# Optimization experiments

Hardware: AMD Instinct MI355X
Metric: run time of the kernel (lower is better)

The kernel has to match this reference:

```python
import jax, jax.numpy as jnp
import numpy as np

B, N, D = 64, 512, 768


def setup_inputs() -> dict:
    key = jax.random.key(0)
    k = jax.random.split(key, 7)
    x = jax.random.normal(k[0], (B, N, D), dtype=jnp.float32)
    adj = jax.random.normal(k[1], (B, N, N), dtype=jnp.float32)
    # additive BERT-style mask: 0 for valid tokens, -10000 for padding
    lengths = jax.random.randint(k[2], (B,), N // 2, N + 1)
    valid = jnp.arange(N)[None, :] < lengths[:, None]          # [B, N]
    mask = jnp.where(valid, 0.0, -10000.0).astype(jnp.float32).reshape(B, 1, 1, N)
    roots_label = (jax.random.uniform(k[3], (B, N)) < 0.1).astype(jnp.float32)
    root_mask = valid.astype(jnp.int32)
    w_root = jax.random.normal(k[4], (D,), dtype=jnp.float32) / np.sqrt(D)
    b_root = jnp.zeros((), dtype=jnp.float32)
    return {"x": x, "adj": adj, "mask": mask, "roots_label": roots_label,
            "root_mask": root_mask, "w_root": w_root, "b_root": b_root}


def _matrix_tree_multi(scores, root):
    # scores: [B,N,N], root: [B,N]
    A = jnp.exp(scores)
    R = jnp.exp(root)
    L = jnp.sum(A, axis=1)                     # column sums (torch dim=1)
    LL = jnp.zeros_like(A).at[:, jnp.arange(A.shape[1]), jnp.arange(A.shape[1])].set(L + R) - A
    # equivalent to diag(L) - A + diag(R); keep diag of -A zeroed by set:
    LL = (jnp.apply_along_axis(jnp.diag, 1, np.zeros((1,))) if False else LL)  # no-op
    LL = jax.vmap(jnp.diag)(L + R) - A + jax.vmap(jnp.diag)(jnp.diagonal(A, axis1=1, axis2=2))
    # Recompute cleanly to match torch exactly: LL = diag(L) - A + diag(R)
    LL = jax.vmap(jnp.diag)(L) - A + jax.vmap(jnp.diag)(R)
    LL_inv = jnp.linalg.inv(LL)                # [B,N,N]
    LL_inv_diag = jnp.diagonal(LL_inv, axis1=1, axis2=2)   # [B,N]
    d0 = R * LL_inv_diag                       # root marginals [B,N]
    tmp1 = A * LL_inv_diag[:, None, :]         # A[i,j] * diag[j]
    tmp2 = A * jnp.swapaxes(LL_inv, 1, 2)      # A[i,j] * LL_inv[j,i]
    d = tmp1 - tmp2                            # edge marginals [B,N,N]
    return d, d0


def reference(x, adj, mask, roots_label, root_mask, w_root, b_root):
    root = jnp.einsum("bnd,d->bn", x, w_root) + b_root          # [B,N]
    m = mask[:, 0] / -10000.0                                    # [B,1,N], 0 valid / 1 pad
    root = jnp.maximum(root - m[:, 0, :] * 50.0, -40.0)
    scores = adj - m * 50.0 - jnp.swapaxes(m, 1, 2) * 50.0
    scores = jnp.maximum(scores, -40.0)
    d, d0 = _matrix_tree_multi(scores, root)
    # BCE root loss
    active = root_mask.reshape(-1) == 1
    labels = jnp.where(active, roots_label.reshape(-1), 0.0).astype(jnp.float32)
    logits = jnp.clip(d0.reshape(-1), 1e-5, 1.0 - 1e-5).astype(jnp.float32)
    bce = -(labels * jnp.log(logits) + (1.0 - labels) * jnp.log(1.0 - logits))
    loss_root = jnp.mean(bce * root_mask.reshape(-1).astype(jnp.float32))
    # attention = d^T with padded key columns zeroed
    attn = jnp.swapaxes(d, 1, 2)
    pad = jnp.broadcast_to(m.astype(bool), scores.shape)         # [B,N,N]
    attn = jnp.where(pad, 0.0, attn)
    context = jnp.matmul(attn, x)                                # [B,N,D]
    return context, d, loss_root
```

## Files before the change

kernel.cpp:

```cpp
#include <hip/hip_runtime.h>
#include <cstdint>
#include <cstddef>

#define BB 64
#define NN 512
#define DD 768
#define KB 64
#define NSTEP (NN/KB)

typedef __bf16 bf16x8 __attribute__((ext_vector_type(8)));
typedef float f32x4 __attribute__((ext_vector_type(4)));
typedef unsigned short us8 __attribute__((ext_vector_type(8)));
typedef double f64x4 __attribute__((ext_vector_type(4)));
typedef double f64x2 __attribute__((ext_vector_type(2)));

__device__ __forceinline__ float aval(float adjv, float mi, float mj) {
    return expf(fmaxf(adjv - 50.f * (mi + mj), -40.f));
}

__device__ __forceinline__ unsigned short f2bf(float v) {
    union { float f; unsigned int u; } c; c.f = v;
    return (unsigned short)((c.u + 0x7fffu + ((c.u >> 16) & 1u)) >> 16);
}
__device__ __forceinline__ float bf2f(unsigned short h) {
    union { unsigned int u; float f; } c; c.u = ((unsigned int)h) << 16;
    return c.f;
}

__device__ __forceinline__ void gl_lds16(const void* g, void* l) {
    __builtin_amdgcn_global_load_lds((const __attribute__((address_space(1))) unsigned int*)g,
                                     (__attribute__((address_space(3))) unsigned int*)l, 16, 0, 0);
}

__global__ void k_root(const float* __restrict__ x, const float* __restrict__ mask,
                       const float* __restrict__ w, const float* __restrict__ br,
                       float* __restrict__ R) {
    int wave = threadIdx.x >> 6, lane = threadIdx.x & 63;
    int row = blockIdx.x * 4 + wave;
    const float* xr = x + (size_t)row * DD;
    float s = 0.f;
#pragma unroll
    for (int k = 0; k < DD / 64; ++k) s += xr[k * 64 + lane] * w[k * 64 + lane];
    for (int off = 32; off; off >>= 1) s += __shfl_down(s, off, 64);
    if (lane == 0) {
        float m = mask[row] * -1e-4f;
        float rv = fmaxf(s + br[0] - 50.f * m, -40.f);
        R[row] = expf(rv);
    }
}

__global__ void k_colsum(const float* __restrict__ adj, const float* __restrict__ mask,
                         double* __restrict__ Lp) {
    int b = blockIdx.x, chunk = blockIdx.y;
    int j = threadIdx.x;
    float mj = mask[b * NN + j] * -1e-4f;
    const float* ab = adj + (size_t)b * NN * NN;
    double acc = 0.0;
    int i0 = chunk * 128;
    for (int i = i0; i < i0 + 128; ++i) {
        float mi = mask[b * NN + i] * -1e-4f;
        acc += (double)aval(ab[(size_t)i * NN + j], mi, mj);
    }
    Lp[((size_t)b * 4 + chunk) * NN + j] = acc;
}

template <typename T>
__global__ void k_build(const float* __restrict__ adj, const float* __restrict__ mask,
                        const float* __restrict__ R, const double* __restrict__ Lp,
                        T* __restrict__ M) {
    int b = blockIdx.x >> 9;
    int r = blockIdx.x & 511;
    int c = threadIdx.x;
    float mr = mask[b * NN + r] * -1e-4f;
    float mc = mask[b * NN + c] * -1e-4f;
    size_t idx = ((size_t)b * NN + r) * NN + c;
    float a = aval(adj[idx], mr, mc);
    T v;
    if (r == c) {
        const double* lp = Lp + (size_t)b * 4 * NN;
        double L = lp[c] + lp[NN + c] + lp[2 * NN + c] + lp[3 * NN + c];
        v = (T)(L - (double)a + (double)R[b * NN + c]);
    } else {
        v = (T)(-a);
    }
    M[idx] = v;
}

template <typename T>
__global__ void k_savecol(const T* __restrict__ M, T* __restrict__ Cb, int k0) {
    int t = threadIdx.x;
    int c = t & 63, rr = t >> 6;
    int row = blockIdx.x * 4 + rr;
    int b = row >> 9, i = row & 511;
    Cb[(size_t)row * KB + c] = M[((size_t)b * NN + i) * NN + k0 + c];
}

template <typename T>
__global__ void k_invblk(const T* __restrict__ M, T* __restrict__ Bb, int k0) {
    __shared__ double pr[KB];
    __shared__ double fv[KB];
    __shared__ double pvt;
    int b = blockIdx.x;
    int r = threadIdx.x & 63, q = threadIdx.x >> 6;
    double a[16];
    const T* Mb = M + ((size_t)b * NN + k0) * NN + k0;
#pragma unroll
    for (int c = 0; c < 16; ++c) a[c] = (double)Mb[(size_t)r * NN + q * 16 + c];
    for (int k = 0; k < KB; ++k) {
        int kq = k >> 4, kc = k & 15;
        if (r == k && q == kq) pvt = a[kc];
        __syncthreads();
        double ip = 1.0 / pvt;
        if (r == k) {
#pragma unroll
            for (int c = 0; c < 16; ++c) a[c] *= ip;
            if (q == kq) a[kc] = ip;
#pragma unroll
            for (int c = 0; c < 16; ++c) pr[q * 16 + c] = a[c];
        }
        if (r != k && q == kq) fv[r] = a[kc];
        __syncthreads();
        if (r != k) {
            double f = fv[r];
#pragma unroll
            for (int c = 0; c < 16; ++c) a[c] -= f * pr[q * 16 + c];
            if (q == kq) a[kc] = -f * ip;
        }
        __syncthreads();
    }
    T* Bo = Bb + (size_t)b * KB * KB;
#pragma unroll
    for (int c = 0; c < 16; ++c) Bo[r * KB + q * 16 + c] = (T)a[c];
}

__global__ __launch_bounds__(256) void k_piv_mfma(double* __restrict__ M,
                                                  const double* __restrict__ Bb, int step) {
    __shared__ double Ms[64][66];
    int o = blockIdx.x;
    int g = (o & 7) * 64 + (o >> 3);
    int b = g >> 3, jt = g & 7;
    int t = threadIdx.x, w = t >> 6, l = t & 63;
    double* Mb = M + (size_t)b * NN * NN;
    double* Pr = Mb + (size_t)(step * 64) * NN;
    const double* Bi = Bb + (size_t)b * KB * KB;
    if (jt == step) {
        for (int i = 0; i < 16; ++i) {
            int c = i * 256 + t;
            int row = c >> 6, col = c & 63;
            Pr[(size_t)row * NN + step * 64 + col] = Bi[row * 64 + col];
        }
        return;
    }
    const double* Mg = Pr + jt * 64;
    for (int i = 0; i < 8; ++i) {
        int c = i * 256 + t;
        int row = c >> 5, ch = c & 31;
        f64x2 v = *(const f64x2*)(Mg + (size_t)row * NN + ch * 2);
        Ms[row][ch * 2] = v[0]; Ms[row][ch * 2 + 1] = v[1];
    }
    __syncthreads();
    int lr = l & 15, lg = l >> 4;
    double a[16];
#pragma unroll
    for (int kk = 0; kk < 16; ++kk) a[kk] = Bi[(w * 16 + lr) * 64 + kk * 4 + lg];
    double* Og = Pr + (size_t)(w * 16) * NN + jt * 64;
#pragma unroll
    for (int cf = 0; cf < 4; ++cf) {
        f64x4 acc = {0., 0., 0., 0.};
#pragma unroll
        for (int kk = 0; kk < 16; ++kk)
            acc = __builtin_amdgcn_mfma_f64_16x16x4f64(a[kk], Ms[kk * 4 + lg][cf * 16 + lr], acc, 0, 0, 0);
#pragma unroll
        for (int r = 0; r < 4; ++r) Og[(size_t)(lg + 4 * r) * NN + cf * 16 + lr] = acc[r];
    }
}

__global__ __launch_bounds__(256) void k_upd2(double* __restrict__ M,
                                              const double* __restrict__ Bb, int step) {
    __shared__ double Ts[64][66];
    int o = blockIdx.x;
    int g = (o & 7) * 112 + (o >> 3);
    int b = g / 14;
    int x = g % 14;
    int it = x >> 1, half = x & 1;
    if (it >= step) ++it;
    int t = threadIdx.x, w = t >> 6, l = t & 63;
    double* Mb = M + (size_t)b * NN * NN;
    {
        const double* Cg = Mb + (size_t)(it * 64) * NN + step * 64;
        for (int i = 0; i < 8; ++i) {
            int c = i * 256 + t;
            int row = c >> 5, ch = c & 31;
            f64x2 v = *(const f64x2*)(Cg + (size_t)row * NN + ch * 2);
            Ts[row][ch * 2] = -v[0]; Ts[row][ch * 2 + 1] = -v[1];
        }
    }
    __syncthreads();
    int lr = l & 15, lg = l >> 4;
    double a[16];
#pragma unroll
    for (int kk = 0; kk < 16; ++kk) a[kk] = Ts[w * 16 + lr][kk * 4 + lg];
    __syncthreads();
    int nj = half ? 3 : 4;
    for (int jj = 0; jj < nj; ++jj) {
        int jtidx = half ? 4 + jj : jj;
        int jt = (jtidx < step) ? jtidx : jtidx + 1;
        const double* Rg = Mb + (size_t)(step * 64) * NN + jt * 64;
        for (int i = 0; i < 8; ++i) {
            int c = i * 256 + t;
            int row = c >> 5, ch = c & 31;
            f64x2 v = *(const f64x2*)(Rg + (size_t)row * NN + ch * 2);
            Ts[row][ch * 2] = v[0]; Ts[row][ch * 2 + 1] = v[1];
        }
        __syncthreads();
        double* Og = Mb + (size_t)(it * 64 + w * 16) * NN + jt * 64;
#pragma unroll
        for (int cf = 0; cf < 4; ++cf) {
            int c0 = cf * 16 + lr;
            f64x4 acc;
#pragma unroll
            for (int r = 0; r < 4; ++r) acc[r] = Og[(size_t)(lg + 4 * r) * NN + c0];
#pragma unroll
            for (int kk = 0; kk < 16; ++kk)
                acc = __builtin_amdgcn_mfma_f64_16x16x4f64(a[kk], Ts[kk * 4 + lg][c0], acc, 0, 0, 0);
#pragma unroll
            for (int r = 0; r < 4; ++r) Og[(size_t)(lg + 4 * r) * NN + c0] = acc[r];
        }
        __syncthreads();
    }
    if (half) {
        const double* Bi = Bb + (size_t)b * KB * KB;
        for (int i = 0; i < 8; ++i) {
            int c = i * 256 + t;
            int row = c >> 5, ch = c & 31;
            f64x2 v = *(const f64x2*)(Bi + row * 64 + ch * 2);
            Ts[row][ch * 2] = v[0]; Ts[row][ch * 2 + 1] = v[1];
        }
        __syncthreads();
        double* Og = Mb + (size_t)(it * 64 + w * 16) * NN + step * 64;
#pragma unroll
        for (int cf = 0; cf < 4; ++cf) {
            int c0 = cf * 16 + lr;
            f64x4 acc = {0., 0., 0., 0.};
#pragma unroll
            for (int kk = 0; kk < 16; ++kk)
                acc = __builtin_amdgcn_mfma_f64_16x16x4f64(a[kk], Ts[kk * 4 + lg][c0], acc, 0, 0, 0);
#pragma unroll
            for (int r = 0; r < 4; ++r) Og[(size_t)(lg + 4 * r) * NN + c0] = acc[r];
        }
    }
}

template <typename T>
__global__ void k_pivrows(T* __restrict__ M, const T* __restrict__ Bb, int k0) {
    __shared__ double Bi[KB][KB];
    __shared__ double Mt[KB][KB + 1];
    int b = blockIdx.x, jt = blockIdx.y * 64;
    const T* Bo = Bb + (size_t)b * KB * KB;
    T* Mb = M + ((size_t)b * NN + k0) * NN;
    int t = threadIdx.x;
    for (int e = t; e < KB * KB; e += 256) {
        int rr = e >> 6, cc = e & 63;
        Bi[rr][cc] = (double)Bo[e];
        Mt[rr][cc] = (double)Mb[(size_t)rr * NN + jt + cc];
    }
    __syncthreads();
    if (blockIdx.y == (unsigned)(k0 >> 6)) {
        for (int e = t; e < KB * KB; e += 256) {
            int rr = e >> 6, cc = e & 63;
            Mb[(size_t)rr * NN + jt + cc] = (T)Bi[rr][cc];
        }
        return;
    }
    int tx = t & 15, ty = t >> 4;
    double acc[4][4] = {};
    for (int k = 0; k < KB; ++k) {
        double av[4], bv[4];
#pragma unroll
        for (int u = 0; u < 4; ++u) { av[u] = Bi[ty * 4 + u][k]; bv[u] = Mt[k][tx * 4 + u]; }
#pragma unroll
        for (int u = 0; u < 4; ++u)
#pragma unroll
            for (int v = 0; v < 4; ++v) acc[u][v] += av[u] * bv[v];
    }
#pragma unroll
    for (int u = 0; u < 4; ++u)
#pragma unroll
        for (int v = 0; v < 4; ++v)
            Mb[(size_t)(ty * 4 + u) * NN + jt + tx * 4 + v] = (T)acc[u][v];
}

template <typename T>
__global__ void k_update(T* __restrict__ M, const T* __restrict__ Cb, int k0) {
    int step = k0 >> 6;
    int it = blockIdx.y;
    if (it == step) return;
    int b = blockIdx.x, jt = blockIdx.z;
    __shared__ double Ct[KB][KB + 1];
    __shared__ double Rt[KB][KB + 1];
    int t = threadIdx.x;
    const T* Cbb = Cb + ((size_t)b * NN + it * 64) * KB;
    const T* Rb  = M + ((size_t)b * NN + k0) * NN + jt * 64;
    for (int e = t; e < KB * KB; e += 256) {
        int rr = e >> 6, cc = e & 63;
        Ct[rr][cc] = (double)Cbb[(size_t)rr * KB + cc];
        Rt[rr][cc] = (double)Rb[(size_t)rr * NN + cc];
    }
    __syncthreads();
    int tx = t & 15, ty = t >> 4;
    double acc[4][4] = {};
    for (int k = 0; k < KB; ++k) {
        double av[4], bv[4];
#pragma unroll
        for (int u = 0; u < 4; ++u) { av[u] = Ct[ty * 4 + u][k]; bv[u] = Rt[k][tx * 4 + u]; }
#pragma unroll
        for (int u = 0; u < 4; ++u)
#pragma unroll
            for (int v = 0; v < 4; ++v) acc[u][v] += av[u] * bv[v];
    }
    T* Mo = M + ((size_t)b * NN + it * 64) * NN + jt * 64;
    bool blockcol = (jt == step);
#pragma unroll
    for (int u = 0; u < 4; ++u) {
        int row = ty * 4 + u;
#pragma unroll
        for (int v = 0; v < 4; ++v) {
            int col = tx * 4 + v;
            double val = (double)Mo[(size_t)row * NN + col] - acc[u][v];
            if (blockcol) val -= Ct[row][col];
            Mo[(size_t)row * NN + col] = (T)val;
        }
    }
}

template <typename T>
__global__ void k_dgloss(const T* __restrict__ M, const float* __restrict__ R,
                         const float* __restrict__ rlab, const int* __restrict__ rmask,
                         double* __restrict__ Dg, float* __restrict__ lossp) {
    int idx = blockIdx.x * 256 + threadIdx.x;
    int b = idx >> 9, n = idx & 511;
    double xv = (double)M[((size_t)b * NN + n) * NN + n];
    Dg[idx] = xv;
    float d0 = R[idx] * (float)xv;
    float lg = fminf(fmaxf(d0, 1e-5f), 1.f - 1e-5f);
    float rm = (float)rmask[idx];
    float lab = (rmask[idx] == 1) ? rlab[idx] : 0.f;
    float bce = -(lab * logf(lg) + (1.f - lab) * logf(1.f - lg));
    __shared__ double sm[256];
    sm[threadIdx.x] = (double)(bce * rm);
    __syncthreads();
    for (int s = 128; s; s >>= 1) {
        if (threadIdx.x < s) sm[threadIdx.x] += sm[threadIdx.x + s];
        __syncthreads();
    }
    if (threadIdx.x == 0) lossp[blockIdx.x] = (float)sm[0];
}

__global__ void k_lossfin(const float* __restrict__ lossp, float* __restrict__ outv) {
    __shared__ double sm[128];
    sm[threadIdx.x] = (double)lossp[threadIdx.x];
    __syncthreads();
    for (int s = 64; s; s >>= 1) {
        if (threadIdx.x < s) sm[threadIdx.x] += sm[threadIdx.x + s];
        __syncthreads();
    }
    if (threadIdx.x == 0) outv[0] = (float)(sm[0] / (double)(BB * NN));
}

template <typename T>
__global__ void k_d(const T* __restrict__ M, const double* __restrict__ Dg,
                    const float* __restrict__ adj, const float* __restrict__ mask,
                    float* __restrict__ dout) {
    int b = blockIdx.x, i0 = blockIdx.y * 64, j0 = blockIdx.z * 64;
    __shared__ double Xt[64][65];
    int t = threadIdx.x, ii = t & 63, jj0 = t >> 6;
    const T* Mb = M + (size_t)b * NN * NN;
    for (int jj = jj0; jj < 64; jj += 4)
        Xt[jj][ii] = (double)Mb[(size_t)(j0 + jj) * NN + i0 + ii];
    __syncthreads();
    int jc = t & 63, ir0 = t >> 6;
    float mj = mask[b * NN + j0 + jc] * -1e-4f;
    double dg = Dg[b * NN + j0 + jc];
    const float* ab = adj + (size_t)b * NN * NN;
    float* db = dout + (size_t)b * NN * NN;
    for (int ir = ir0; ir < 64; ir += 4) {
        int i = i0 + ir;
        float mi = mask[b * NN + i] * -1e-4f;
        float a = aval(ab[(size_t)i * NN + j0 + jc], mi, mj);
        db[(size_t)i * NN + j0 + jc] = a * (float)(dg - Xt[jc][ir]);
    }
}

template <typename T>
__global__ void k_d2(const T* __restrict__ M, const double* __restrict__ Dg,
                     const float* __restrict__ adj, const float* __restrict__ mask,
                     float* __restrict__ dout,
                     unsigned short* __restrict__ ATh, unsigned short* __restrict__ ATl) {
    int b = blockIdx.x, i0 = blockIdx.y * 64, j0 = blockIdx.z * 64;
    __shared__ float Xt[64][65];
    __shared__ float dt[64][65];
    int t = threadIdx.x, ii = t & 63, jj0 = t >> 6;
    const T* Mb = M + (size_t)b * NN * NN;
    for (int jj = jj0; jj < 64; jj += 4)
        Xt[jj][ii] = (float)Mb[(size_t)(j0 + jj) * NN + i0 + ii];
    __syncthreads();
    int jc = t & 63, ir0 = t >> 6;
    float mj = mask[b * NN + j0 + jc] * -1e-4f;
    double dg = Dg[b * NN + j0 + jc];
    const float* ab = adj + (size_t)b * NN * NN;
    float* db = dout + (size_t)b * NN * NN;
    for (int ir = ir0; ir < 64; ir += 4) {
        int i = i0 + ir;
        float mi = mask[b * NN + i] * -1e-4f;
        float a = aval(ab[(size_t)i * NN + j0 + jc], mi, mj);
        float v = a * (float)(dg - (double)Xt[jc][ir]);
        db[(size_t)i * NN + j0 + jc] = v;
        dt[ir][jc] = v;
    }
    __syncthreads();
    int ql = t >> 2, kq = t & 3;
    us8 vh0, vh1, vl0, vl1;
#pragma unroll
    for (int u = 0; u < 16; ++u) {
        int k = kq * 16 + u;
        float mk = mask[b * NN + i0 + k] * -1e-4f;
        float v = (mk > 0.5f) ? 0.f : dt[k][ql];
        unsigned short h = f2bf(v);
        unsigned short lo = f2bf(v - bf2f(h));
        if (u < 8) { vh0[u] = h; vl0[u] = lo; } else { vh1[u - 8] = h; vl1[u - 8] = lo; }
    }
    size_t ao = ((size_t)b * NN + j0 + ql) * NN + i0 + kq * 16;
    *(us8*)&ATh[ao] = vh0; *(us8*)&ATh[ao + 8] = vh1;
    *(us8*)&ATl[ao] = vl0; *(us8*)&ATl[ao + 8] = vl1;
}

__global__ void k_cvt_x(const float* __restrict__ x,
                        unsigned short* __restrict__ XTh, unsigned short* __restrict__ XTl) {
    int b = blockIdx.x, k0 = blockIdx.y * 64, c0 = blockIdx.z * 64;
    __shared__ float xs[64][65];
    int t = threadIdx.x;
#pragma unroll
    for (int rep = 0; rep < 16; ++rep) {
        int e = rep * 256 + t;
        int row = e >> 6, col = e & 63;
        xs[row][col] = x[((size_t)b * NN + k0 + row) * DD + c0 + col];
    }
    __syncthreads();
    int cl = t >> 2, kq = t & 3;
    us8 vh0, vh1, vl0, vl1;
#pragma unroll
    for (int u = 0; u < 16; ++u) {
        int k = kq * 16 + u;
        float v = xs[k][cl];
        unsigned short h = f2bf(v);
        unsigned short lo = f2bf(v - bf2f(h));
        if (u < 8) { vh0[u] = h; vl0[u] = lo; } else { vh1[u - 8] = h; vl1[u - 8] = lo; }
    }
    size_t ao = ((size_t)b * DD + c0 + cl) * NN + k0 + kq * 16;
    *(us8*)&XTh[ao] = vh0; *(us8*)&XTh[ao + 8] = vh1;
    *(us8*)&XTl[ao] = vl0; *(us8*)&XTl[ao + 8] = vl1;
}

__global__ __launch_bounds__(256) void k_ctx5(const unsigned short* __restrict__ ATh,
                                              const unsigned short* __restrict__ ATl,
                                              const unsigned short* __restrict__ XTh,
                                              const unsigned short* __restrict__ XTl,
                                              float* __restrict__ ctx) {
    __shared__ __align__(16) unsigned short ABs[2][128 * 64];
    __shared__ __align__(16) unsigned short Xs[2][128 * 64];
    int o = blockIdx.x;
    int g = (o & 7) * 192 + (o >> 3);
    int b = g / 24;
    int rem = g % 24;
    int bm = (rem / 6) * 128, bn = (rem % 6) * 128;
    int t = threadIdx.x, wid = t >> 6, lane = t & 63;
    f32x4 acc[4][4];
#pragma unroll
    for (int i = 0; i < 4; ++i)
#pragma unroll
        for (int j = 0; j < 4; ++j) acc[i][j] = (f32x4){0.f, 0.f, 0.f, 0.f};

    const unsigned short* Agh = ATh + ((size_t)b * NN + bm) * NN;
    const unsigned short* Agl = ATl + ((size_t)b * NN + bm) * NN;
    const unsigned short* Xgh = XTh + ((size_t)b * DD + bn) * NN;
    const unsigned short* Xgl = XTl + ((size_t)b * DD + bn) * NN;

    int m0 = (wid >> 1) * 64, n0 = (wid & 1) * 64;
    int kc = lane >> 4;

    auto STAGE = [&](int kt, int buf) {
        int ki = kt * 32;
#pragma unroll
        for (int it2 = 0; it2 < 4; ++it2) {
            int chunk = it2 * 256 + wid * 64 + lane;
            int row = chunk >> 3;
            int gs = (chunk & 7) ^ (row & 7);
            const unsigned short* s = (gs < 4) ? Agh + (size_t)row * NN + ki + gs * 8
                                               : Agl + (size_t)row * NN + ki + (gs - 4) * 8;
            gl_lds16(s, &ABs[buf][(it2 * 256 + wid * 64) * 8]);
        }
#pragma unroll
        for (int it2 = 0; it2 < 4; ++it2) {
            int chunk = it2 * 256 + wid * 64 + lane;
            int row = chunk >> 3;
            int gs = (chunk & 7) ^ (row & 7);
            const unsigned short* s = (gs < 4) ? Xgh + (size_t)row * NN + ki + gs * 8
                                               : Xgl + (size_t)row * NN + ki + (gs - 4) * 8;
            gl_lds16(s, &Xs[buf][(it2 * 256 + wid * 64) * 8]);
        }
    };

    STAGE(0, 0);
    int cur = 0;
    for (int kt = 0; kt < 16; ++kt) {
        if (kt + 1 < 16) {
            STAGE(kt + 1, cur ^ 1);
            asm volatile("s_waitcnt vmcnt(8)" ::: "memory");
        } else {
            asm volatile("s_waitcnt vmcnt(0)" ::: "memory");
        }
        __builtin_amdgcn_s_barrier();
        bf16x8 ah[4], al[4], xh[4], xl[4];
#pragma unroll
        for (int f = 0; f < 4; ++f) {
            int ar = m0 + f * 16 + (lane & 15);
            ah[f] = *(const bf16x8*)&ABs[cur][(ar * 8 + (kc ^ (ar & 7))) * 8];
            al[f] = *(const bf16x8*)&ABs[cur][(ar * 8 + ((kc | 4) ^ (ar & 7))) * 8];
            int br = n0 + f * 16 + (lane & 15);
            xh[f] = *(const bf16x8*)&Xs[cur][(br * 8 + (kc ^ (br & 7))) * 8];
            xl[f] = *(const bf16x8*)&Xs[cur][(br * 8 + ((kc | 4) ^ (br & 7))) * 8];
        }
#pragma unroll
        for (int fm = 0; fm < 4; ++fm)
#pragma unroll
            for (int fn = 0; fn < 4; ++fn) {
                acc[fm][fn] = __builtin_amdgcn_mfma_f32_16x16x32_bf16(ah[fm], xh[fn], acc[fm][fn], 0, 0, 0);
                acc[fm][fn] = __builtin_amdgcn_mfma_f32_16x16x32_bf16(ah[fm], xl[fn], acc[fm][fn], 0, 0, 0);
                acc[fm][fn] = __builtin_amdgcn_mfma_f32_16x16x32_bf16(al[fm], xh[fn], acc[fm][fn], 0, 0, 0);
            }
        __builtin_amdgcn_s_barrier();
        cur ^= 1;
    }
    float* cb = ctx + ((size_t)b * NN + bm + m0) * DD + bn + n0;
#pragma unroll
    for (int fm = 0; fm < 4; ++fm)
#pragma unroll
        for (int fn = 0; fn < 4; ++fn)
#pragma unroll
            for (int r = 0; r < 4; ++r) {
                int row = fm * 16 + (lane >> 4) * 4 + r;
                int col = fn * 16 + (lane & 15);
                cb[(size_t)row * DD + col] = acc[fm][fn][r];
            }
}

__global__ void k_ctx(const float* __restrict__ dmat, const float* __restrict__ x,
                      const float* __restrict__ mask, float* __restrict__ ctx) {
    int b = blockIdx.x, i0 = blockIdx.y * 64, c0 = blockIdx.z * 64;
    __shared__ float At[32][65];
    __shared__ float Xl[32][65];
    int t = threadIdx.x;
    int tx = t & 15, ty = t >> 4;
    float acc[4][4] = {};
    const float* db = dmat + (size_t)b * NN * NN;
    const float* xb = x + (size_t)b * NN * DD;
    int li = t & 63, lk = t >> 6;
    for (int kt = 0; kt < NN; kt += 32) {
#pragma unroll
        for (int rep = 0; rep < 8; ++rep) {
            int kk = lk + rep * 4;
            float mk = mask[b * NN + kt + kk] * -1e-4f;
            float v = db[(size_t)(kt + kk) * NN + i0 + li];
            At[kk][li] = (mk > 0.5f) ? 0.f : v;
            Xl[kk][li] = xb[(size_t)(kt + kk) * DD + c0 + li];
        }
        __syncthreads();
        for (int kk = 0; kk < 32; ++kk) {
            float av[4], bv[4];
#pragma unroll
            for (int u = 0; u < 4; ++u) { av[u] = At[kk][ty * 4 + u]; bv[u] = Xl[kk][tx * 4 + u]; }
#pragma unroll
            for (int u = 0; u < 4; ++u)
#pragma unroll
                for (int v = 0; v < 4; ++v) acc[u][v] += av[u] * bv[v];
        }
        __syncthreads();
    }
    float* cb = ctx + (size_t)b * NN * DD;
#pragma unroll
    for (int u = 0; u < 4; ++u)
#pragma unroll
        for (int v = 0; v < 4; ++v)
            cb[(size_t)(i0 + ty * 4 + u) * DD + c0 + tx * 4 + v] = acc[u][v];
}

template <typename T>
static void run_old(const float* x, const float* adj, const float* mask,
                    const float* rlab, const int* rmask, const float* w, const float* br,
                    float* ctx, float* dmat, float* lossout,
                    char* ws, hipStream_t stream) {
    size_t off = 0;
    T* M  = (T*)(ws + off); off += (size_t)BB * NN * NN * sizeof(T);
    T* Cb = (T*)(ws + off); off += (size_t)BB * NN * KB * sizeof(T);
    T* Bb = (T*)(ws + off); off += (size_t)BB * KB * KB * sizeof(T);
    double* Lp = (double*)(ws + off); off += (size_t)BB * 4 * NN * 8;
    float* Rf  = (float*)(ws + off);  off += (size_t)BB * NN * 4;
    double* Dg = (double*)(ws + off); off += (size_t)BB * NN * 8;
    float* lossp = (float*)(ws + off);

    k_root<<<BB * NN / 4, 256, 0, stream>>>(x, mask, w, br, Rf);
    k_colsum<<<dim3(BB, 4), 512, 0, stream>>>(adj, mask, Lp);
    k_build<T><<<BB * NN, 512, 0, stream>>>(adj, mask, Rf, Lp, M);
    for (int s = 0; s < NSTEP; ++s) {
        int k0 = s * KB;
        k_savecol<T><<<BB * NN / 4, 256, 0, stream>>>(M, Cb, k0);
        k_invblk<T><<<BB, 256, 0, stream>>>(M, Bb, k0);
        k_pivrows<T><<<dim3(BB, 8), 256, 0, stream>>>(M, Bb, k0);
        k_update<T><<<dim3(BB, 8, 8), 256, 0, stream>>>(M, Cb, k0);
    }
    k_dgloss<T><<<BB * NN / 256, 256, 0, stream>>>(M, Rf, rlab, rmask, Dg, lossp);
    k_lossfin<<<1, 128, 0, stream>>>(lossp, lossout);
    k_d<T><<<dim3(BB, 8, 8), 256, 0, stream>>>(M, Dg, adj, mask, dmat);
    k_ctx<<<dim3(BB, 8, 12), 256, 0, stream>>>(dmat, x, mask, ctx);
}

static void run_new(const float* x, const float* adj, const float* mask,
                    const float* rlab, const int* rmask, const float* w, const float* br,
                    float* ctx, float* dmat, float* lossout,
                    char* ws, hipStream_t stream) {
    size_t off = 0;
    double* M  = (double*)(ws + off); off += (size_t)BB * NN * NN * 8;
    double* Cb = (double*)(ws + off); off += (size_t)BB * NN * KB * 8;
    double* Bb = (double*)(ws + off); off += (size_t)BB * KB * KB * 8;
    double* Lp = (double*)(ws + off); off += (size_t)BB * 4 * NN * 8;
    float* Rf  = (float*)(ws + off);  off += (size_t)BB * NN * 4;
    double* Dg = (double*)(ws + off); off += (size_t)BB * NN * 8;
    float* lossp = (float*)(ws + off); off += 4096;
    unsigned short* ATh = (unsigned short*)(ws + off); off += (size_t)BB * NN * NN * 2;
    unsigned short* ATl = (unsigned short*)(ws + off); off += (size_t)BB * NN * NN * 2;
    unsigned short* XTh = (unsigned short*)(ws);
    unsigned short* XTl = (unsigned short*)(ws + (size_t)BB * DD * NN * 2);
    (void)Cb;

    k_root<<<BB * NN / 4, 256, 0, stream>>>(x, mask, w, br, Rf);
    k_colsum<<<dim3(BB, 4), 512, 0, stream>>>(adj, mask, Lp);
    k_build<double><<<BB * NN, 512, 0, stream>>>(adj, mask, Rf, Lp, M);
    for (int s = 0; s < NSTEP; ++s) {
        k_invblk<double><<<BB, 256, 0, stream>>>(M, Bb, s * KB);
        k_piv_mfma<<<512, 256, 0, stream>>>(M, Bb, s);
        k_upd2<<<896, 256, 0, stream>>>(M, Bb, s);
    }
    k_dgloss<double><<<BB * NN / 256, 256, 0, stream>>>(M, Rf, rlab, rmask, Dg, lossp);
    k_lossfin<<<1, 128, 0, stream>>>(lossp, lossout);
    k_d2<double><<<dim3(BB, 8, 8), 256, 0, stream>>>(M, Dg, adj, mask, dmat, ATh, ATl);
    k_cvt_x<<<dim3(BB, 8, 12), 256, 0, stream>>>(x, XTh, XTl);
    k_ctx5<<<1536, 256, 0, stream>>>(ATh, ATl, XTh, XTl, ctx);
}

extern "C" void kernel_launch(void* const* d_in, const int* in_sizes, int n_in,
                              void* d_out, int out_size, void* d_ws, size_t ws_size,
                              hipStream_t stream) {
    const float* x    = (const float*)d_in[0];
    const float* adj  = (const float*)d_in[1];
    const float* mask = (const float*)d_in[2];
    const float* rlab = (const float*)d_in[3];
    const int*   rmask= (const int*)d_in[4];
    const float* w    = (const float*)d_in[5];
    const float* br   = (const float*)d_in[6];
    float* out = (float*)d_out;
    float* ctx = out;
    float* dmat = out + (size_t)BB * NN * DD;
    float* lossout = dmat + (size_t)BB * NN * NN;
    char* ws = (char*)d_ws;

    size_t base = (size_t)BB * NN * NN * 8 + (size_t)BB * NN * KB * 8 + (size_t)BB * KB * KB * 8
                + (size_t)BB * 4 * NN * 8 + (size_t)BB * NN * 4 + (size_t)BB * NN * 8 + 4096;
    size_t need_new = base + (size_t)BB * NN * NN * 4;
    if (ws_size >= need_new)
        run_new(x, adj, mask, rlab, rmask, w, br, ctx, dmat, lossout, ws, stream);
    else if (ws_size >= base)
        run_old<double>(x, adj, mask, rlab, rmask, w, br, ctx, dmat, lossout, ws, stream);
    else
        run_old<float>(x, adj, mask, rlab, rmask, w, br, ctx, dmat, lossout, ws, stream);
}
```

Baseline: 1.177 ms.

## Fuse colsum into build, pair row tiles in update kernel, reorder ctx MFMAs

Merges the column-sum and matrix-build kernels into one pass over adj that writes -A and accumulates column sums for the diagonal, so adj is read once instead of twice. The trailing update kernel now handles two row tiles per block and double-buffers the pivot-row tiles through registers and LDS, which halves pivot-row reloads and overlaps global loads with MFMA work. It also folds the inverse-block product into the same loop. The context GEMM's inner MFMA loop is split into three passes so independent accumulators are interleaved. The update change cuts grid size from 896 to 256 blocks, which reduces parallelism and raises register pressure.

```diff
diff --git a/kernel.cpp b/kernel.cpp
--- a/kernel.cpp
+++ b/kernel.cpp
@@ -46,6 +46,36 @@
         float m = mask[row] * -1e-4f;
         float rv = fmaxf(s + br[0] - 50.f * m, -40.f);
         R[row] = expf(rv);
+    }
+}
+
+__global__ __launch_bounds__(512) void k_build2(const float* __restrict__ adj,
+                                                const float* __restrict__ mask,
+                                                const float* __restrict__ R,
+                                                double* __restrict__ M) {
+    __shared__ double ls[4][128];
+    int b = blockIdx.x >> 2;
+    int c0 = (blockIdx.x & 3) * 128;
+    int t = threadIdx.x;
+    int col = c0 + (t & 127), rg4 = t >> 7;
+    float mc = mask[b * NN + col] * -1e-4f;
+    const float* ab = adj + (size_t)b * NN * NN;
+    double* Mb = M + (size_t)b * NN * NN;
+    double sum = 0.0;
+    for (int row = rg4; row < NN; row += 4) {
+        float mr = mask[b * NN + row] * -1e-4f;
+        float a = aval(ab[(size_t)row * NN + col], mr, mc);
+        sum += (double)a;
+        Mb[(size_t)row * NN + col] = -(double)a;
+    }
+    ls[rg4][t & 127] = sum;
+    __syncthreads();
+    if (t < 128) {
+        int j = c0 + t;
+        double L = ls[0][t] + ls[1][t] + ls[2][t] + ls[3][t];
+        float mj = mask[b * NN + j] * -1e-4f;
+        float a = aval(ab[(size_t)j * NN + j], mj, mj);
+        Mb[(size_t)j * NN + j] = L - (double)a + (double)R[b * NN + j];
     }
 }
 
@@ -175,78 +205,106 @@
     }
 }
 
-__global__ __launch_bounds__(256) void k_upd2(double* __restrict__ M,
+__global__ __launch_bounds__(256) void k_upd3(double* __restrict__ M,
                                               const double* __restrict__ Bb, int step) {
-    __shared__ double Ts[64][66];
+    __shared__ double Rb[2][64][66];
     int o = blockIdx.x;
-    int g = (o & 7) * 112 + (o >> 3);
-    int b = g / 14;
-    int x = g % 14;
-    int it = x >> 1, half = x & 1;
-    if (it >= step) ++it;
+    int g = (o & 7) * 32 + (o >> 3);
+    int b = g >> 2, p = g & 3;
+    int itA = 2 * p, itB = 2 * p + 1;
+    bool hasB = (itB < 7);
+    if (itA >= step) ++itA;
+    if (hasB && itB >= step) ++itB;
     int t = threadIdx.x, w = t >> 6, l = t & 63;
+    int lr = l & 15, lg = l >> 4;
     double* Mb = M + (size_t)b * NN * NN;
+    const double* Pr = Mb + (size_t)(step * 64) * NN;
+    const double* Bi = Bb + (size_t)b * KB * KB;
+
     {
-        const double* Cg = Mb + (size_t)(it * 64) * NN + step * 64;
+        const double* CgA = Mb + (size_t)(itA * 64) * NN + step * 64;
         for (int i = 0; i < 8; ++i) {
-            int c = i * 256 + t;
-            int row = c >> 5, ch = c & 31;
-            f64x2 v = *(const f64x2*)(Cg + (size_t)row * NN + ch * 2);
-            Ts[row][ch * 2] = -v[0]; Ts[row][ch * 2 + 1] = -v[1];
-        }
-    }
-    __syncthreads();
-    int lr = l & 15, lg = l >> 4;
-    double a[16];
-#pragma unroll
-    for (int kk = 0; kk < 16; ++kk) a[kk] = Ts[w * 16 + lr][kk * 4 + lg];
-    __syncthreads();
-    int nj = half ? 3 : 4;
-    for (int jj = 0; jj < nj; ++jj) {
-        int jtidx = half ? 4 + jj : jj;
-        int jt = (jtidx < step) ? jtidx : jtidx + 1;
-        const double* Rg = Mb + (size_t)(step * 64) * NN + jt * 64;
+            int c = i * 256 + t, row = c >> 5, ch = c & 31;
+            f64x2 v = *(const f64x2*)(CgA + (size_t)row * NN + ch * 2);
+            Rb[0][row][ch * 2] = -v[0]; Rb[0][row][ch * 2 + 1] = -v[1];
+        }
+        if (hasB) {
+            const double* CgB = Mb + (size_t)(itB * 64) * NN + step * 64;
+            for (int i = 0; i < 8; ++i) {
+                int c = i * 256 + t, row = c >> 5, ch = c & 31;
+                f64x2 v = *(const f64x2*)(CgB + (size_t)row * NN + ch * 2);
+                Rb[1][row][ch * 2] = -v[0]; Rb[1][row][ch * 2 + 1] = -v[1];
+            }
+        }
+    }
+    __syncthreads();
+    double aA[16], aB[16];
+#pragma unroll
+    for (int kk = 0; kk < 16; ++kk) aA[kk] = Rb[0][w * 16 + lr][kk * 4 + lg];
+    if (hasB) {
+#pragma unroll
+        for (int kk = 0; kk < 16; ++kk) aB[kk] = Rb[1][w * 16 + lr][kk * 4 + lg];
+    }
+    __syncthreads();
+
+    f64x2 rg[8];
+    auto LOADP = [&](int jj) {
+        const double* src; size_t stride;
+        if (jj < 7) { int jt = (jj < step) ? jj : jj + 1; src = Pr + jt * 64; stride = NN; }
+        else { src = Bi; stride = 64; }
         for (int i = 0; i < 8; ++i) {
-            int c = i * 256 + t;
-            int row = c >> 5, ch = c & 31;
-            f64x2 v = *(const f64x2*)(Rg + (size_t)row * NN + ch * 2);
-            Ts[row][ch * 2] = v[0]; Ts[row][ch * 2 + 1] = v[1];
-        }
-        __syncthreads();
-        double* Og = Mb + (size_t)(it * 64 + w * 16) * NN + jt * 64;
+            int c = i * 256 + t, row = c >> 5, ch = c & 31;
+            rg[i] = *(const f64x2*)(src + (size_t)row * stride + ch * 2);
+        }
+    };
+    auto WRITEP = [&](int buf) {
+        for (int i = 0; i < 8; ++i) {
+            int c = i * 256 + t, row = c >> 5, ch = c & 31;
+            Rb[buf][row][ch * 2] = rg[i][0]; Rb[buf][row][ch * 2 + 1] = rg[i][1];
+        }
+    };
+
+    LOADP(0);
+    WRITEP(0);
+    __syncthreads();
+    int cur = 0;
+    for (int jj = 0; jj < 8; ++jj) {
+        if (jj + 1 < 8) LOADP(jj + 1);
+        int jt = (jj < 7) ? ((jj < step) ? jj : jj + 1) : step;
+        bool init = (jj < 7);
+        double* OgA = Mb + (size_t)(itA * 64 + w * 16) * NN + jt * 64;
+        double* OgB = Mb + (size_t)(itB * 64 + w * 16) * NN + jt * 64;
 #pragma unroll
         for (int cf = 0; cf < 4; ++cf) {
             int c0 = cf * 16 + lr;
-            f64x4 acc;
-#pragma unroll
-            for (int r = 0; r < 4; ++r) acc[r] = Og[(size_t)(lg + 4 * r) * NN + c0];
+            f64x4 accA = {0., 0., 0., 0.};
+            if (init) {
+#pragma unroll
+                for (int r = 0; r < 4; ++r) accA[r] = OgA[(size_t)(lg + 4 * r) * NN + c0];
+            }
 #pragma unroll
             for (int kk = 0; kk < 16; ++kk)
-                acc = __builtin_amdgcn_mfma_f64_16x16x4f64(a[kk], Ts[kk * 4 + lg][c0], acc, 0, 0, 0);
-#pragma unroll
-            for (int r = 0; r < 4; ++r) Og[(size_t)(lg + 4 * r) * NN + c0] = acc[r];
+                accA = __builtin_amdgcn_mfma_f64_16x16x4f64(aA[kk], Rb[cur][kk * 4 + lg][c0], accA, 0, 0, 0);
+#pragma unroll
+            for (int r = 0; r < 4; ++r) OgA[(size_t)(lg + 4 * r) * NN + c0] = accA[r];
+            if (hasB) {
+                f64x4 accB = {0., 0., 0., 0.};
+                if (init) {
+#pragma unroll
+                    for (int r = 0; r < 4; ++r) accB[r] = OgB[(size_t)(lg + 4 * r) * NN + c0];
+                }
+#pragma unroll
+                for (int kk = 0; kk < 16; ++kk)
+                    accB = __builtin_amdgcn_mfma_f64_16x16x4f64(aB[kk], Rb[cur][kk * 4 + lg][c0], accB, 0, 0, 0);
+#pragma unroll
+                for (int r = 0; r < 4; ++r) OgB[(size_t)(lg + 4 * r) * NN + c0] = accB[r];
+            }
         }
         __syncthreads();
-    }
-    if (half) {
-        const double* Bi = Bb + (size_t)b * KB * KB;
-        for (int i = 0; i < 8; ++i) {
-            int c = i * 256 + t;
-            int row = c >> 5, ch = c & 31;
-            f64x2 v = *(const f64x2*)(Bi + row * 64 + ch * 2);
-            Ts[row][ch * 2] = v[0]; Ts[row][ch * 2 + 1] = v[1];
-        }
-        __syncthreads();
-        double* Og = Mb + (size_t)(it * 64 + w * 16) * NN + step * 64;
-#pragma unroll
-        for (int cf = 0; cf < 4; ++cf) {
-            int c0 = cf * 16 + lr;
-            f64x4 acc = {0., 0., 0., 0.};
-#pragma unroll
-            for (int kk = 0; kk < 16; ++kk)
-                acc = __builtin_amdgcn_mfma_f64_16x16x4f64(a[kk], Ts[kk * 4 + lg][c0], acc, 0, 0, 0);
-#pragma unroll
-            for (int r = 0; r < 4; ++r) Og[(size_t)(lg + 4 * r) * NN + c0] = acc[r];
+        if (jj + 1 < 8) {
+            WRITEP(cur ^ 1);
+            __syncthreads();
+            cur ^= 1;
         }
     }
 }
@@ -461,7 +519,7 @@
     *(us8*)&XTl[ao] = vl0; *(us8*)&XTl[ao + 8] = vl1;
 }
 
-__global__ __launch_bounds__(256) void k_ctx5(const unsigned short* __restrict__ ATh,
+__global__ __launch_bounds__(256) void k_ctx6(const unsigned short* __restrict__ ATh,
                                               const unsigned short* __restrict__ ATl,
                                               const unsigned short* __restrict__ XTh,
                                               const unsigned short* __restrict__ XTl,
@@ -533,11 +591,18 @@
 #pragma unroll
         for (int fm = 0; fm < 4; ++fm)
 #pragma unroll
-            for (int fn = 0; fn < 4; ++fn) {
+            for (int fn = 0; fn < 4; ++fn)
                 acc[fm][fn] = __builtin_amdgcn_mfma_f32_16x16x32_bf16(ah[fm], xh[fn], acc[fm][fn], 0, 0, 0);
+#pragma unroll
+        for (int fm = 0; fm < 4; ++fm)
+#pragma unroll
+            for (int fn = 0; fn < 4; ++fn)
                 acc[fm][fn] = __builtin_amdgcn_mfma_f32_16x16x32_bf16(ah[fm], xl[fn], acc[fm][fn], 0, 0, 0);
+#pragma unroll
+        for (int fm = 0; fm < 4; ++fm)
+#pragma unroll
+            for (int fn = 0; fn < 4; ++fn)
                 acc[fm][fn] = __builtin_amdgcn_mfma_f32_16x16x32_bf16(al[fm], xh[fn], acc[fm][fn], 0, 0, 0);
-            }
         __builtin_amdgcn_s_barrier();
         cur ^= 1;
     }
@@ -640,21 +705,20 @@
     unsigned short* ATl = (unsigned short*)(ws + off); off += (size_t)BB * NN * NN * 2;
     unsigned short* XTh = (unsigned short*)(ws);
     unsigned short* XTl = (unsigned short*)(ws + (size_t)BB * DD * NN * 2);
-    (void)Cb;
+    (void)Cb; (void)Lp;
 
     k_root<<<BB * NN / 4, 256, 0, stream>>>(x, mask, w, br, Rf);
-    k_colsum<<<dim3(BB, 4), 512, 0, stream>>>(adj, mask, Lp);
-    k_build<double><<<BB * NN, 512, 0, stream>>>(adj, mask, Rf, Lp, M);
+    k_build2<<<BB * 4, 512, 0, stream>>>(adj, mask, Rf, M);
     for (int s = 0; s < NSTEP; ++s) {
         k_invblk<double><<<BB, 256, 0, stream>>>(M, Bb, s * KB);
         k_piv_mfma<<<512, 256, 0, stream>>>(M, Bb, s);
-        k_upd2<<<896, 256, 0, stream>>>(M, Bb, s);
+        k_upd3<<<256, 256, 0, stream>>>(M, Bb, s);
     }
     k_dgloss<double><<<BB * NN / 256, 256, 0, stream>>>(M, Rf, rlab, rmask, Dg, lossp);
     k_lossfin<<<1, 128, 0, stream>>>(lossp, lossout);
     k_d2<double><<<dim3(BB, 8, 8), 256, 0, stream>>>(M, Dg, adj, mask, dmat, ATh, ATl);
     k_cvt_x<<<dim3(BB, 8, 12), 256, 0, stream>>>(x, XTh, XTl);
-    k_ctx5<<<1536, 256, 0, stream>>>(ATh, ATl, XTh, XTl, ctx);
+    k_ctx6<<<1536, 256, 0, stream>>>(ATh, ATl, XTh, XTl, ctx);
 }
 
 extern "C" void kernel_launch(void* const* d_in, const int* in_sizes, int n_in,
```

Result: slower. 1.325 ms (+12.6%).
